# Optimization experiments

Measured on AMD Instinct MI355X. Metric: run time of the kernel, lower is better.

Reference implementation:

```python
import jax, jax.numpy as jnp
import numpy as np

N = 50000
E = 800000
NEG_SLOPE = 0.2


def gatv2_layer(x, src, dst, Wl, Wr, att, bias, heads, ch):
    # x: [N, Fin]; Wl/Wr: [Fin, heads*ch]; att: [heads, ch]; bias: [heads*ch]
    xl = (x @ Wl).reshape(N, heads, ch)  # source transform
    xr = (x @ Wr).reshape(N, heads, ch)  # target transform
    e = xl[src] + xr[dst]                              # [E, H, C]
    s = jnp.einsum('ehc,hc->eh', jax.nn.leaky_relu(e, NEG_SLOPE), att)  # [E, H]
    # scatter-softmax over incoming edges of each target node
    smax = jax.ops.segment_max(s, dst, num_segments=N)  # [N, H]
    ex = jnp.exp(s - smax[dst])
    denom = jax.ops.segment_sum(ex, dst, num_segments=N)
    alpha = ex / denom[dst]                             # [E, H]
    out = jax.ops.segment_sum(xl[src] * alpha[..., None], dst, num_segments=N)  # [N, H, C]
    return out.reshape(N, heads * ch) + bias


def setup_inputs() -> dict:
    key = jax.random.key(0)
    ks = jax.random.split(key, 12)
    x = jax.random.normal(ks[0], (N, 128), dtype=jnp.float32)
    edge_index = jax.random.randint(ks[1], (2, E), 0, N, dtype=jnp.int64)
    edge_attr = jax.random.normal(ks[2], (E, 16), dtype=jnp.float32)
    s1 = 1.0 / np.sqrt(128.0)
    # layer 1: 128 -> 64, heads=2 (concat -> 128)
    Wl1 = jax.random.normal(ks[3], (128, 128), dtype=jnp.float32) * s1
    Wr1 = jax.random.normal(ks[4], (128, 128), dtype=jnp.float32) * s1
    att1 = jax.random.normal(ks[5], (2, 64), dtype=jnp.float32) * 0.1
    b1 = jnp.zeros((128,), dtype=jnp.float32)
    # layer 2: 128 -> 128, heads=1
    Wl2 = jax.random.normal(ks[6], (128, 128), dtype=jnp.float32) * s1
    Wr2 = jax.random.normal(ks[7], (128, 128), dtype=jnp.float32) * s1
    att2 = jax.random.normal(ks[8], (1, 128), dtype=jnp.float32) * 0.1
    b2 = jnp.zeros((128,), dtype=jnp.float32)
    return {"x": x, "edge_index": edge_index, "edge_attr": edge_attr,
            "Wl1": Wl1, "Wr1": Wr1, "att1": att1, "b1": b1,
            "Wl2": Wl2, "Wr2": Wr2, "att2": att2, "b2": b2}


def reference(x, edge_index, edge_attr, Wl1, Wr1, att1, b1, Wl2, Wr2, att2, b2):
    # using_edge_attr=False default path: edge_attr ignored.
    # GATv2Conv default add_self_loops=True
    loops = jnp.arange(N, dtype=edge_index.dtype)
    src = jnp.concatenate([edge_index[0], loops])
    dst = jnp.concatenate([edge_index[1], loops])
    h = gatv2_layer(x, src, dst, Wl1, Wr1, att1, b1, heads=2, ch=64)
    out = gatv2_layer(h, src, dst, Wl2, Wr2, att2, b2, heads=1, ch=128)
    return out
```

## Files before the change

kernel.cpp:

```cpp
#include <hip/hip_runtime.h>

#define NEG_SLOPE 0.2f
#define NPB 256
#define CHUNK 4096
#define BCAP 5120

typedef _Float16 f16x8 __attribute__((ext_vector_type(8)));
typedef _Float16 f16x4 __attribute__((ext_vector_type(4)));
typedef _Float16 f16x2 __attribute__((ext_vector_type(2)));
typedef float    f32x4 __attribute__((ext_vector_type(4)));
typedef float    f32x8 __attribute__((ext_vector_type(8)));

#if defined(__has_builtin)
#if __has_builtin(__builtin_amdgcn_fdot2)
#define HAVE_FDOT2 1
#endif
#if __has_builtin(__builtin_amdgcn_exp2f)
#define FEXP2(x) __builtin_amdgcn_exp2f(x)
#endif
#endif
#ifndef FEXP2
#define FEXP2(x) exp2f(x)
#endif

__device__ __forceinline__ f32x8 cvt8(f16x8 v) {
    return __builtin_convertvector(v, f32x8);
}

template <int CTRL>
__device__ __forceinline__ float dpp_add(float v) {
    int o = __builtin_amdgcn_update_dpp(0, __builtin_bit_cast(int, v),
                                        CTRL, 0xF, 0xF, true);
    return v + __builtin_bit_cast(float, o);
}

__global__ __launch_bounds__(256) void k1_prep_bucket_kernel(
    const float* __restrict__ W0, const float* __restrict__ W1,
    const float* __restrict__ W2, const float* __restrict__ W3,
    _Float16* __restrict__ wt,
    const float* __restrict__ x, _Float16* __restrict__ xh,
    _Float16* __restrict__ xlo, int total,
    const int* __restrict__ ei, int* __restrict__ gcursor,
    int2* __restrict__ staging, int E, int B0)
{
    __shared__ int2 pairs[CHUNK];
    __shared__ int bh[256], bbase[256], exb[256], scn[256];
    int t = threadIdx.x;
    int bid = blockIdx.x;

    if (bid < B0) {
        bh[t] = 0;
        __syncthreads();
        int base = bid * CHUNK;
        int srcv[16], dstv[16], rb[16];
#pragma unroll
        for (int j = 0; j < 16; j++) {
            int e = base + t + j * 256;
            if (e < E) {
                int d = ei[E + e];
                srcv[j] = ei[e];
                dstv[j] = d;
                int bk = d >> 8;
                int r = atomicAdd(&bh[bk], 1);
                rb[j] = (r << 8) | bk;
            } else rb[j] = -1;
        }
        __syncthreads();
        int v = bh[t];
        scn[t] = v;
        __syncthreads();
        for (int off = 1; off < 256; off <<= 1) {
            int u = (t >= off) ? scn[t - off] : 0;
            __syncthreads();
            scn[t] += u;
            __syncthreads();
        }
        int ex = scn[t] - v;
        int tot = scn[255];
        exb[t] = ex;
        if (v) bbase[t] = t * BCAP + atomicAdd(&gcursor[t], v);
        __syncthreads();
#pragma unroll
        for (int j = 0; j < 16; j++) {
            if (rb[j] >= 0) {
                int bk = rb[j] & 255, r = rb[j] >> 8;
                pairs[exb[bk] + r] = make_int2(srcv[j], dstv[j]);
            }
        }
        __syncthreads();
        for (int i = t; i < tot; i += 256) {
            int2 p = pairs[i];
            int bk = p.y >> 8;
            staging[bbase[bk] + (i - exb[bk])] = p;
        }
    } else if (bid < B0 + 256) {
        int idx = (bid - B0) * 256 + t;
        int m = idx >> 14;
        int k = (idx >> 7) & 127;
        int n = idx & 127;
        const float* W = (m == 0) ? W0 : (m == 1) ? W1 : (m == 2) ? W2 : W3;
        wt[m * 16384 + n * 128 + k] = (_Float16)W[k * 128 + n];
    } else {
        int i = (bid - B0 - 256) * 256 + t;
        if (i * 2 < total) {
            float2 f = *(const float2*)(x + (size_t)i * 2);
            _Float16 h0 = (_Float16)f.x, h1 = (_Float16)f.y;
            _Float16 l0 = (_Float16)(f.x - (float)h0), l1 = (_Float16)(f.y - (float)h1);
            *(f16x2*)(xh  + (size_t)i * 2) = (f16x2){h0, h1};
            *(f16x2*)(xlo + (size_t)i * 2) = (f16x2){l0, l1};
        }
    }
}

__device__ __forceinline__ void gemm_body(
    const _Float16* __restrict__ Ahi, const _Float16* __restrict__ Alo,
    const _Float16* __restrict__ Wt, _Float16* __restrict__ C, int N,
    int bx, _Float16* ldsW)
{
    const int tid = threadIdx.x;
    const int wave = tid >> 6;
    const int lane = tid & 63;
    const int mrow = lane & 15;
    const int quad = lane >> 4;
    const int rbase = bx * 128 + wave * 32;

    const int sn = tid >> 1, shf = tid & 1;
    float4 stg[8];
    {
        const float4* g = (const float4*)(Wt + sn * 128 + shf * 64);
#pragma unroll
        for (int j = 0; j < 8; j++) stg[j] = g[j];
    }

    f16x8 ah[2][4], al[2][4];
#pragma unroll
    for (int rt = 0; rt < 2; rt++) {
        int r = rbase + rt * 16 + mrow;
        if (r > N - 1) r = N - 1;
        const _Float16* pa = Ahi + (size_t)r * 128 + quad * 8;
        const _Float16* pl = Alo + (size_t)r * 128 + quad * 8;
#pragma unroll
        for (int s = 0; s < 4; s++) {
            ah[rt][s] = *(const f16x8*)(pa + s * 32);
            al[rt][s] = *(const f16x8*)(pl + s * 32);
        }
    }

    {
        float4* d = (float4*)&ldsW[sn * 136 + shf * 64];
#pragma unroll
        for (int j = 0; j < 8; j++) d[j] = stg[j];
    }

    f32x4 acc[2][8];
#pragma unroll
    for (int rt = 0; rt < 2; rt++)
#pragma unroll
        for (int c = 0; c < 8; c++) acc[rt][c] = (f32x4){0.f, 0.f, 0.f, 0.f};

    __syncthreads();

#pragma unroll
    for (int s = 0; s < 4; s++) {
#pragma unroll
        for (int c = 0; c < 8; c++) {
            f16x8 bw = *(const f16x8*)&ldsW[(c * 16 + mrow) * 136 + s * 32 + quad * 8];
            acc[0][c] = __builtin_amdgcn_mfma_f32_16x16x32_f16(ah[0][s], bw, acc[0][c], 0, 0, 0);
            acc[0][c] = __builtin_amdgcn_mfma_f32_16x16x32_f16(al[0][s], bw, acc[0][c], 0, 0, 0);
            acc[1][c] = __builtin_amdgcn_mfma_f32_16x16x32_f16(ah[1][s], bw, acc[1][c], 0, 0, 0);
            acc[1][c] = __builtin_amdgcn_mfma_f32_16x16x32_f16(al[1][s], bw, acc[1][c], 0, 0, 0);
        }
    }

#pragma unroll
    for (int rt = 0; rt < 2; rt++)
#pragma unroll
        for (int i = 0; i < 4; i++) {
            int r = rbase + rt * 16 + quad * 4 + i;
            if (r < N) {
                _Float16* cr = C + (size_t)r * 128 + mrow;
#pragma unroll
                for (int c = 0; c < 8; c++) cr[c * 16] = (_Float16)acc[rt][c][i];
            }
        }
}

__global__ __launch_bounds__(256) void gemm_f16_kernel(
    const _Float16* __restrict__ Ahi, const _Float16* __restrict__ Alo,
    const _Float16* __restrict__ Wt0, const _Float16* __restrict__ Wt1,
    _Float16* __restrict__ Cl, _Float16* __restrict__ Cr, int N)
{
    __shared__ _Float16 ldsW[128 * 136];
    gemm_body(Ahi, Alo, blockIdx.y ? Wt1 : Wt0, blockIdx.y ? Cr : Cl, N,
              blockIdx.x, ldsW);
}

__global__ __launch_bounds__(256) void k2_sort_gemm_kernel(
    const int2* __restrict__ staging, const int* __restrict__ gcursor,
    int* __restrict__ start, int* __restrict__ deg,
    int* __restrict__ sorted_src, int N, int NBv,
    const _Float16* __restrict__ Ahi, const _Float16* __restrict__ Alo,
    const _Float16* __restrict__ Wt0, const _Float16* __restrict__ Wt1,
    _Float16* __restrict__ Cl, _Float16* __restrict__ Cr, int gx)
{
    __shared__ _Float16 ldsW[128 * 136];
    int bx = blockIdx.x;
    if (bx < NBv) {
        int* lhist = (int*)ldsW;
        int* lscan = lhist + 256;
        int* lcur  = lhist + 512;
        int b = bx, t = threadIdx.x;
        int r0 = b * BCAP;
        int r1 = r0 + gcursor[b];
        lhist[t] = 0;
        __syncthreads();
        for (int i = r0 + t; i < r1; i += 256) atomicAdd(&lhist[staging[i].y & 255], 1);
        __syncthreads();
        int v = lhist[t];
        lscan[t] = v;
        __syncthreads();
        for (int off = 1; off < 256; off <<= 1) {
            int u = (t >= off) ? lscan[t - off] : 0;
            __syncthreads();
            lscan[t] += u;
            __syncthreads();
        }
        int excl = lscan[t] - v;
        int node = b * NPB + t;
        if (node < N) { start[node] = r0 + excl; deg[node] = v; }
        lcur[t] = excl;
        __syncthreads();
        for (int i = r0 + t; i < r1; i += 256) {
            int2 p = staging[i];
            int rank = atomicAdd(&lcur[p.y & 255], 1);
            sorted_src[r0 + rank] = p.x << 8;
        }
    } else {
        int gb = bx - NBv;
        int y = (gb >= gx) ? 1 : 0;
        int gxi = y ? gb - gx : gb;
        gemm_body(Ahi, Alo, y ? Wt1 : Wt0, y ? Cr : Cl, N, gxi, ldsW);
    }
}

template <int H, bool BFOUT>
__global__ __launch_bounds__(256) void gat_fused_kernel(
    const _Float16* __restrict__ xl, const _Float16* __restrict__ xr,
    const float* __restrict__ att, const float* __restrict__ bias,
    const int* __restrict__ start, const int* __restrict__ deg,
    const int* __restrict__ sorted_src,
    float* __restrict__ outf, _Float16* __restrict__ oh,
    _Float16* __restrict__ ol, int N, int npairs)
{
    const int wid = threadIdx.x >> 6;
    int p = blockIdx.x * 4 + wid;
    if (p >= npairs) return;
    const int stride = gridDim.x * 4;
    const int lane = threadIdx.x & 63;
    const int g  = lane >> 4;
    const int hl = lane & 15;
    const unsigned hl16 = (unsigned)hl * 16;
    const _Float16 NS = (_Float16)NEG_SLOPE;
    const float L2E = 1.44269504f;

    float4 at0 = *(const float4*)(att + hl * 8);
    float4 at1 = *(const float4*)(att + hl * 8 + 4);
    float4 bi0 = *(const float4*)(bias + hl * 8);
    float4 bi1 = *(const float4*)(bias + hl * 8 + 4);
#if defined(HAVE_FDOT2)
    f16x2 av0 = {(_Float16)(at0.x * L2E), (_Float16)(at0.y * L2E)};
    f16x2 av1 = {(_Float16)(at0.z * L2E), (_Float16)(at0.w * L2E)};
    f16x2 av2 = {(_Float16)(at1.x * L2E), (_Float16)(at1.y * L2E)};
    f16x2 av3 = {(_Float16)(at1.z * L2E), (_Float16)(at1.w * L2E)};
#else
    f32x8 avf = {at0.x * L2E, at0.y * L2E, at0.z * L2E, at0.w * L2E,
                 at1.x * L2E, at1.y * L2E, at1.z * L2E, at1.w * L2E};
#endif

    auto score = [&](f16x8 a_, f16x8 b4_) -> float {
        f16x8 t = a_ + b4_;
        f16x8 u = __builtin_elementwise_max(t, t * NS);
#if defined(HAVE_FDOT2)
        f16x2 u0 = __builtin_shufflevector(u, u, 0, 1);
        f16x2 u1 = __builtin_shufflevector(u, u, 2, 3);
        f16x2 u2 = __builtin_shufflevector(u, u, 4, 5);
        f16x2 u3 = __builtin_shufflevector(u, u, 6, 7);
        return __builtin_amdgcn_fdot2(u0, av0,
               __builtin_amdgcn_fdot2(u1, av1,
               __builtin_amdgcn_fdot2(u2, av2,
               __builtin_amdgcn_fdot2(u3, av3, 0.f, false), false), false), false);
#else
        f32x8 uf = cvt8(u);
        float pp = 0.f;
#pragma unroll
        for (int i = 0; i < 8; i++) pp += uf[i] * avf[i];
        return pp;
#endif
    };

    auto red = [&](float v) -> float {
        v = dpp_add<0xB1>(v);
        v = dpp_add<0x4E>(v);
        v = dpp_add<0x141>(v);
        if (H == 1) v = dpp_add<0x140>(v);
        return v;
    };

    const unsigned cap = (unsigned)(N - 1) << 8;
    auto ldoff = [&](int pos) -> unsigned {
        unsigned v = (unsigned)sorted_src[pos];
        return (v < cap) ? v : cap;
    };
    auto grow = [&](unsigned off) -> f16x8 {
        return *(const f16x8*)((const char*)xl + (size_t)(off + hl16));
    };

    int n0 = 2 * p;
    bool has1 = (n0 + 1) < N;
    int n1 = has1 ? n0 + 1 : n0;
    int s00 = start[n0], M0 = deg[n0] + 1;
    int s01 = start[n1], M1 = deg[n1] + 1;

    for (;;) {
        const int pn = p + stride;
        const bool hn = pn < npairs;
        const int nn0 = hn ? 2 * pn : n0;
        const bool nhas1 = (nn0 + 1) < N;
        const int nn1 = nhas1 ? nn0 + 1 : nn0;
        int ns00 = start[nn0], nM0 = deg[nn0] + 1;
        int ns01 = start[nn1], nM1 = deg[nn1] + 1;

        const f16x8 b40 = *(const f16x8*)(xr + (size_t)n0 * 128 + hl * 8);
        const f16x8 b41 = *(const f16x8*)(xr + (size_t)n1 * 128 + hl * 8);

        const int Mmax = (M0 > M1) ? M0 : M1;
        const int K   = (Mmax + 3) >> 2;
        const int KK  = (K + 1) & ~1;

        f32x8 acc0 = {0.f, 0.f, 0.f, 0.f, 0.f, 0.f, 0.f, 0.f};
        f32x8 acc1 = {0.f, 0.f, 0.f, 0.f, 0.f, 0.f, 0.f, 0.f};
        float den0 = 0.f, den1 = 0.f;

        auto cone = [&](int kk, f16x8 a, f16x8 b4_, int M_, float& den_, f32x8& acc_) {
            float v = red(score(a, b4_));
            float e = (4 * kk + g < M_) ? FEXP2(v) : 0.f;
            den_ += e;
#pragma unroll
            for (int i = 0; i < 8; i++)
                acc_[i] = fmaf((float)a[i], e, acc_[i]);
        };

        unsigned o00 = (g == 0) ? (unsigned)n0 << 8 : ldoff(s00 + g - 1);
        unsigned o01 = (g == 0) ? (unsigned)n1 << 8 : ldoff(s01 + g - 1);
        unsigned o10 = ldoff(s00 + g + 3);
        unsigned o11 = ldoff(s01 + g + 3);
        f16x8 c00 = grow(o00), c01 = grow(o01), c10 = grow(o10), c11 = grow(o11);
        for (int k = 2; k < KK; k += 2) {
            unsigned p00 = ldoff(s00 + 4 * k + g - 1);
            unsigned p01 = ldoff(s01 + 4 * k + g - 1);
            unsigned p10 = ldoff(s00 + 4 * k + g + 3);
            unsigned p11 = ldoff(s01 + 4 * k + g + 3);
            f16x8 d00 = grow(p00), d01 = grow(p01), d10 = grow(p10), d11 = grow(p11);
            cone(k - 2, c00, b40, M0, den0, acc0);
            cone(k - 2, c01, b41, M1, den1, acc1);
            cone(k - 1, c10, b40, M0, den0, acc0);
            cone(k - 1, c11, b41, M1, den1, acc1);
            c00 = d00; c01 = d01; c10 = d10; c11 = d11;
        }
        cone(KK - 2, c00, b40, M0, den0, acc0);
        cone(KK - 2, c01, b41, M1, den1, acc1);
        cone(KK - 1, c10, b40, M0, den0, acc0);
        cone(KK - 1, c11, b41, M1, den1, acc1);

        den0 += __shfl_xor(den0, 16, 64);
        den0 += __shfl_xor(den0, 32, 64);
        den1 += __shfl_xor(den1, 16, 64);
        den1 += __shfl_xor(den1, 32, 64);
#pragma unroll
        for (int i = 0; i < 8; i++) {
            acc0[i] += __shfl_xor(acc0[i], 16, 64);
            acc0[i] += __shfl_xor(acc0[i], 32, 64);
            acc1[i] += __shfl_xor(acc1[i], 16, 64);
            acc1[i] += __shfl_xor(acc1[i], 32, 64);
        }

        const int which = lane >> 4;
        if (which == 0 || (which == 1 && has1)) {
            float inv = 1.0f / (which == 0 ? den0 : den1);
            int nodeo = (which == 0) ? n0 : n1;
            float o[8];
#pragma unroll
            for (int i = 0; i < 8; i++) {
                float a = (which == 0) ? acc0[i] : acc1[i];
                float b = (i < 4) ? ((i == 0) ? bi0.x : (i == 1) ? bi0.y : (i == 2) ? bi0.z : bi0.w)
                                  : ((i == 4) ? bi1.x : (i == 5) ? bi1.y : (i == 6) ? bi1.z : bi1.w);
                o[i] = a * inv + b;
            }
            if (BFOUT) {
                f16x8 hv, lv;
#pragma unroll
                for (int i = 0; i < 8; i++) {
                    _Float16 h = (_Float16)o[i];
                    hv[i] = h;
                    lv[i] = (_Float16)(o[i] - (float)h);
                }
                *(f16x8*)(oh + (size_t)nodeo * 128 + hl * 8) = hv;
                *(f16x8*)(ol + (size_t)nodeo * 128 + hl * 8) = lv;
            } else {
                *(float4*)(outf + (size_t)nodeo * 128 + hl * 8) =
                    make_float4(o[0], o[1], o[2], o[3]);
                *(float4*)(outf + (size_t)nodeo * 128 + hl * 8 + 4) =
                    make_float4(o[4], o[5], o[6], o[7]);
            }
        }

        if (!hn) break;
        p = pn; n0 = nn0; has1 = nhas1; n1 = nn1;
        s00 = ns00; M0 = nM0; s01 = ns01; M1 = nM1;
    }
}

extern "C" void kernel_launch(void* const* d_in, const int* in_sizes, int n_in,
                              void* d_out, int out_size, void* d_ws, size_t ws_size,
                              hipStream_t stream)
{
    const float* x    = (const float*)d_in[0];
    const int*   ei   = (const int*)d_in[1];
    const float* Wl1  = (const float*)d_in[3];
    const float* Wr1  = (const float*)d_in[4];
    const float* att1 = (const float*)d_in[5];
    const float* b1   = (const float*)d_in[6];
    const float* Wl2  = (const float*)d_in[7];
    const float* Wr2  = (const float*)d_in[8];
    const float* att2 = (const float*)d_in[9];
    const float* b2   = (const float*)d_in[10];
    float* out = (float*)d_out;

    const int N  = in_sizes[0] / 128;
    const int E  = in_sizes[1] / 2;
    const int NB = (N + NPB - 1) / NPB;

    const size_t nf = (size_t)N * 128;
    _Float16* xlf  = (_Float16*)d_ws;
    _Float16* xrf  = xlf + nf;
    _Float16* ah   = xrf + nf;
    _Float16* al   = ah + nf;
    _Float16* wt   = al + nf;
    int* gcursor   = (int*)(wt + 4 * 16384);
    int* start     = gcursor + 256;
    int* deg       = start + N;
    size_t stgoff  = ((size_t)(deg + N) + 7) & ~(size_t)7;
    int2* staging  = (int2*)stgoff;
    int* sorted_src = (int*)(staging + (size_t)NB * BCAP);

    const int grid_chunk = (E + CHUNK - 1) / CHUNK;
    const int npairs     = (N + 1) / 2;
    int node_grid        = (npairs + 3) / 4;
    if (node_grid > 2048) node_grid = 2048;
    const int gemm_gx    = (N + 127) / 128;
    const int split_grid = (int)((nf / 2 + 255) / 256);

    hipMemsetAsync(gcursor, 0, 256 * sizeof(int), stream);

    k1_prep_bucket_kernel<<<grid_chunk + 256 + split_grid, 256, 0, stream>>>(
        Wl1, Wr1, Wl2, Wr2, wt, x, ah, al, (int)nf,
        ei, gcursor, staging, E, grid_chunk);

    k2_sort_gemm_kernel<<<NB + 2 * gemm_gx, 256, 0, stream>>>(
        staging, gcursor, start, deg, sorted_src, N, NB,
        ah, al, wt + 0 * 16384, wt + 1 * 16384, xlf, xrf, gemm_gx);

    gat_fused_kernel<2, true><<<node_grid, 256, 0, stream>>>(
        xlf, xrf, att1, b1, start, deg, sorted_src, nullptr, ah, al, N, npairs);

    gemm_f16_kernel<<<dim3(gemm_gx, 2), 256, 0, stream>>>(
        ah, al, wt + 2 * 16384, wt + 3 * 16384, xlf, xrf, N);
    gat_fused_kernel<1, false><<<node_grid, 256, 0, stream>>>(
        xlf, xrf, att2, b2, start, deg, sorted_src, out, nullptr, nullptr, N, npairs);
}
```

Baseline: 265.6 us.

## Merge all stages into one persistent cooperative kernel with grid syncs

Replaces the memset and five separate launches with a single cooperative mega-kernel sized to full occupancy. The stages (weight/input split, bucketing plus first GEMM, per-bucket sort, layer-1 attention, second GEMM, layer-2 attention) run as grid-strided loops separated by grid.sync. Shared memory becomes a union so one allocation serves every stage. The aim is to remove launch gaps and tail effects between kernels, at the cost of grid-wide barriers, a register cap from launch_bounds(256,4), and dropping the next-pair start/deg prefetch in the attention loop.

```diff
diff --git a/kernel.cpp b/kernel.cpp
--- a/kernel.cpp
+++ b/kernel.cpp
@@ -1,4 +1,6 @@
 #include <hip/hip_runtime.h>
+#include <hip/hip_cooperative_groups.h>
+namespace cg = cooperative_groups;
 
 #define NEG_SLOPE 0.2f
 #define NPB 256
@@ -6,7 +8,6 @@
 #define BCAP 5120
 
 typedef _Float16 f16x8 __attribute__((ext_vector_type(8)));
-typedef _Float16 f16x4 __attribute__((ext_vector_type(4)));
 typedef _Float16 f16x2 __attribute__((ext_vector_type(2)));
 typedef float    f32x4 __attribute__((ext_vector_type(4)));
 typedef float    f32x8 __attribute__((ext_vector_type(8)));
@@ -23,10 +24,6 @@
 #define FEXP2(x) exp2f(x)
 #endif
 
-__device__ __forceinline__ f32x8 cvt8(f16x8 v) {
-    return __builtin_convertvector(v, f32x8);
-}
-
 template <int CTRL>
 __device__ __forceinline__ float dpp_add(float v) {
     int o = __builtin_amdgcn_update_dpp(0, __builtin_bit_cast(int, v),
@@ -34,81 +31,60 @@
     return v + __builtin_bit_cast(float, o);
 }
 
-__global__ __launch_bounds__(256) void k1_prep_bucket_kernel(
-    const float* __restrict__ W0, const float* __restrict__ W1,
-    const float* __restrict__ W2, const float* __restrict__ W3,
-    _Float16* __restrict__ wt,
-    const float* __restrict__ x, _Float16* __restrict__ xh,
-    _Float16* __restrict__ xlo, int total,
-    const int* __restrict__ ei, int* __restrict__ gcursor,
-    int2* __restrict__ staging, int E, int B0)
-{
-    __shared__ int2 pairs[CHUNK];
-    __shared__ int bh[256], bbase[256], exb[256], scn[256];
+union SharedU {
+    struct { int2 pairs[CHUNK]; int bh[256]; int bbase[256]; int exb[256]; int scn[256]; } b;
+    _Float16 w[128 * 136];
+    struct { int lhist[256]; int lscan[256]; int lcur[256]; } s;
+};
+
+__device__ __forceinline__ void bucket_chunk_body(
+    SharedU& L, const int* __restrict__ ei, int* __restrict__ gcursor,
+    int2* __restrict__ staging, int E, int bid)
+{
     int t = threadIdx.x;
-    int bid = blockIdx.x;
-
-    if (bid < B0) {
-        bh[t] = 0;
-        __syncthreads();
-        int base = bid * CHUNK;
-        int srcv[16], dstv[16], rb[16];
-#pragma unroll
-        for (int j = 0; j < 16; j++) {
-            int e = base + t + j * 256;
-            if (e < E) {
-                int d = ei[E + e];
-                srcv[j] = ei[e];
-                dstv[j] = d;
-                int bk = d >> 8;
-                int r = atomicAdd(&bh[bk], 1);
-                rb[j] = (r << 8) | bk;
-            } else rb[j] = -1;
-        }
-        __syncthreads();
-        int v = bh[t];
-        scn[t] = v;
-        __syncthreads();
-        for (int off = 1; off < 256; off <<= 1) {
-            int u = (t >= off) ? scn[t - off] : 0;
-            __syncthreads();
-            scn[t] += u;
-            __syncthreads();
-        }
-        int ex = scn[t] - v;
-        int tot = scn[255];
-        exb[t] = ex;
-        if (v) bbase[t] = t * BCAP + atomicAdd(&gcursor[t], v);
-        __syncthreads();
-#pragma unroll
-        for (int j = 0; j < 16; j++) {
-            if (rb[j] >= 0) {
-                int bk = rb[j] & 255, r = rb[j] >> 8;
-                pairs[exb[bk] + r] = make_int2(srcv[j], dstv[j]);
-            }
-        }
-        __syncthreads();
-        for (int i = t; i < tot; i += 256) {
-            int2 p = pairs[i];
-            int bk = p.y >> 8;
-            staging[bbase[bk] + (i - exb[bk])] = p;
-        }
-    } else if (bid < B0 + 256) {
-        int idx = (bid - B0) * 256 + t;
-        int m = idx >> 14;
-        int k = (idx >> 7) & 127;
-        int n = idx & 127;
-        const float* W = (m == 0) ? W0 : (m == 1) ? W1 : (m == 2) ? W2 : W3;
-        wt[m * 16384 + n * 128 + k] = (_Float16)W[k * 128 + n];
-    } else {
-        int i = (bid - B0 - 256) * 256 + t;
-        if (i * 2 < total) {
-            float2 f = *(const float2*)(x + (size_t)i * 2);
-            _Float16 h0 = (_Float16)f.x, h1 = (_Float16)f.y;
-            _Float16 l0 = (_Float16)(f.x - (float)h0), l1 = (_Float16)(f.y - (float)h1);
-            *(f16x2*)(xh  + (size_t)i * 2) = (f16x2){h0, h1};
-            *(f16x2*)(xlo + (size_t)i * 2) = (f16x2){l0, l1};
-        }
+    L.b.bh[t] = 0;
+    __syncthreads();
+    int base = bid * CHUNK;
+    int srcv[16], dstv[16], rb[16];
+#pragma unroll
+    for (int j = 0; j < 16; j++) {
+        int e = base + t + j * 256;
+        if (e < E) {
+            int d = ei[E + e];
+            srcv[j] = ei[e];
+            dstv[j] = d;
+            int bk = d >> 8;
+            int r = atomicAdd(&L.b.bh[bk], 1);
+            rb[j] = (r << 8) | bk;
+        } else rb[j] = -1;
+    }
+    __syncthreads();
+    int v = L.b.bh[t];
+    L.b.scn[t] = v;
+    __syncthreads();
+    for (int off = 1; off < 256; off <<= 1) {
+        int u = (t >= off) ? L.b.scn[t - off] : 0;
+        __syncthreads();
+        L.b.scn[t] += u;
+        __syncthreads();
+    }
+    int ex = L.b.scn[t] - v;
+    int tot = L.b.scn[255];
+    L.b.exb[t] = ex;
+    if (v) L.b.bbase[t] = t * BCAP + atomicAdd(&gcursor[t], v);
+    __syncthreads();
+#pragma unroll
+    for (int j = 0; j < 16; j++) {
+        if (rb[j] >= 0) {
+            int bk = rb[j] & 255, r = rb[j] >> 8;
+            L.b.pairs[L.b.exb[bk] + r] = make_int2(srcv[j], dstv[j]);
+        }
+    }
+    __syncthreads();
+    for (int i = t; i < tot; i += 256) {
+        int2 p = L.b.pairs[i];
+        int bk = p.y >> 8;
+        staging[L.b.bbase[bk] + (i - L.b.exb[bk])] = p;
     }
 }
 
@@ -185,66 +161,41 @@
         }
 }
 
-__global__ __launch_bounds__(256) void gemm_f16_kernel(
-    const _Float16* __restrict__ Ahi, const _Float16* __restrict__ Alo,
-    const _Float16* __restrict__ Wt0, const _Float16* __restrict__ Wt1,
-    _Float16* __restrict__ Cl, _Float16* __restrict__ Cr, int N)
-{
-    __shared__ _Float16 ldsW[128 * 136];
-    gemm_body(Ahi, Alo, blockIdx.y ? Wt1 : Wt0, blockIdx.y ? Cr : Cl, N,
-              blockIdx.x, ldsW);
-}
-
-__global__ __launch_bounds__(256) void k2_sort_gemm_kernel(
-    const int2* __restrict__ staging, const int* __restrict__ gcursor,
+__device__ __forceinline__ void sort_bucket_body(
+    SharedU& L, const int2* __restrict__ staging, const int* __restrict__ gcursor,
     int* __restrict__ start, int* __restrict__ deg,
-    int* __restrict__ sorted_src, int N, int NBv,
-    const _Float16* __restrict__ Ahi, const _Float16* __restrict__ Alo,
-    const _Float16* __restrict__ Wt0, const _Float16* __restrict__ Wt1,
-    _Float16* __restrict__ Cl, _Float16* __restrict__ Cr, int gx)
-{
-    __shared__ _Float16 ldsW[128 * 136];
-    int bx = blockIdx.x;
-    if (bx < NBv) {
-        int* lhist = (int*)ldsW;
-        int* lscan = lhist + 256;
-        int* lcur  = lhist + 512;
-        int b = bx, t = threadIdx.x;
-        int r0 = b * BCAP;
-        int r1 = r0 + gcursor[b];
-        lhist[t] = 0;
-        __syncthreads();
-        for (int i = r0 + t; i < r1; i += 256) atomicAdd(&lhist[staging[i].y & 255], 1);
-        __syncthreads();
-        int v = lhist[t];
-        lscan[t] = v;
-        __syncthreads();
-        for (int off = 1; off < 256; off <<= 1) {
-            int u = (t >= off) ? lscan[t - off] : 0;
-            __syncthreads();
-            lscan[t] += u;
-            __syncthreads();
-        }
-        int excl = lscan[t] - v;
-        int node = b * NPB + t;
-        if (node < N) { start[node] = r0 + excl; deg[node] = v; }
-        lcur[t] = excl;
-        __syncthreads();
-        for (int i = r0 + t; i < r1; i += 256) {
-            int2 p = staging[i];
-            int rank = atomicAdd(&lcur[p.y & 255], 1);
-            sorted_src[r0 + rank] = p.x << 8;
-        }
-    } else {
-        int gb = bx - NBv;
-        int y = (gb >= gx) ? 1 : 0;
-        int gxi = y ? gb - gx : gb;
-        gemm_body(Ahi, Alo, y ? Wt1 : Wt0, y ? Cr : Cl, N, gxi, ldsW);
+    int* __restrict__ sorted_src, int N, int b)
+{
+    int t = threadIdx.x;
+    int r0 = b * BCAP;
+    int r1 = r0 + gcursor[b];
+    L.s.lhist[t] = 0;
+    __syncthreads();
+    for (int i = r0 + t; i < r1; i += 256) atomicAdd(&L.s.lhist[staging[i].y & 255], 1);
+    __syncthreads();
+    int v = L.s.lhist[t];
+    L.s.lscan[t] = v;
+    __syncthreads();
+    for (int off = 1; off < 256; off <<= 1) {
+        int u = (t >= off) ? L.s.lscan[t - off] : 0;
+        __syncthreads();
+        L.s.lscan[t] += u;
+        __syncthreads();
+    }
+    int excl = L.s.lscan[t] - v;
+    int node = b * NPB + t;
+    if (node < N) { start[node] = r0 + excl; deg[node] = v; }
+    L.s.lcur[t] = excl;
+    __syncthreads();
+    for (int i = r0 + t; i < r1; i += 256) {
+        int2 p = staging[i];
+        int rank = atomicAdd(&L.s.lcur[p.y & 255], 1);
+        sorted_src[r0 + rank] = p.x << 8;
     }
 }
 
 template <int H, bool BFOUT>
-__global__ __launch_bounds__(256) void gat_fused_kernel(
+__device__ __forceinline__ void fused_pairs_body(
     const _Float16* __restrict__ xl, const _Float16* __restrict__ xr,
     const float* __restrict__ att, const float* __restrict__ bias,
     const int* __restrict__ start, const int* __restrict__ deg,
@@ -253,9 +204,6 @@
     _Float16* __restrict__ ol, int N, int npairs)
 {
     const int wid = threadIdx.x >> 6;
-    int p = blockIdx.x * 4 + wid;
-    if (p >= npairs) return;
-    const int stride = gridDim.x * 4;
     const int lane = threadIdx.x & 63;
     const int g  = lane >> 4;
     const int hl = lane & 15;
@@ -290,7 +238,7 @@
                __builtin_amdgcn_fdot2(u2, av2,
                __builtin_amdgcn_fdot2(u3, av3, 0.f, false), false), false), false);
 #else
-        f32x8 uf = cvt8(u);
+        f32x8 uf = __builtin_convertvector(u, f32x8);
         float pp = 0.f;
 #pragma unroll
         for (int i = 0; i < 8; i++) pp += uf[i] * avf[i];
@@ -315,20 +263,12 @@
         return *(const f16x8*)((const char*)xl + (size_t)(off + hl16));
     };
 
-    int n0 = 2 * p;
-    bool has1 = (n0 + 1) < N;
-    int n1 = has1 ? n0 + 1 : n0;
-    int s00 = start[n0], M0 = deg[n0] + 1;
-    int s01 = start[n1], M1 = deg[n1] + 1;
-
-    for (;;) {
-        const int pn = p + stride;
-        const bool hn = pn < npairs;
-        const int nn0 = hn ? 2 * pn : n0;
-        const bool nhas1 = (nn0 + 1) < N;
-        const int nn1 = nhas1 ? nn0 + 1 : nn0;
-        int ns00 = start[nn0], nM0 = deg[nn0] + 1;
-        int ns01 = start[nn1], nM1 = deg[nn1] + 1;
+    for (int p = blockIdx.x * 4 + wid; p < npairs; p += gridDim.x * 4) {
+        const int n0 = 2 * p;
+        const bool has1 = (n0 + 1) < N;
+        const int n1 = has1 ? n0 + 1 : n0;
+        const int s00 = start[n0], M0 = deg[n0] + 1;
+        const int s01 = start[n1], M1 = deg[n1] + 1;
 
         const f16x8 b40 = *(const f16x8*)(xr + (size_t)n0 * 128 + hl * 8);
         const f16x8 b41 = *(const f16x8*)(xr + (size_t)n1 * 128 + hl * 8);
@@ -413,11 +353,155 @@
                     make_float4(o[4], o[5], o[6], o[7]);
             }
         }
-
-        if (!hn) break;
-        p = pn; n0 = nn0; has1 = nhas1; n1 = nn1;
-        s00 = ns00; M0 = nM0; s01 = ns01; M1 = nM1;
-    }
+    }
+}
+
+struct MegaArgs {
+    const float *W0, *W1, *W2, *W3;
+    _Float16 *wt;
+    const float *x;
+    _Float16 *xh, *xlo;
+    int total;
+    const int *ei;
+    int *gcursor;
+    int2 *staging;
+    int E, B0;
+    int *start, *deg, *sorted_src;
+    int N, NB, gx, npairs;
+    _Float16 *xlf, *xrf;
+    const float *att1, *b1, *att2, *b2;
+    float *out;
+};
+
+__global__ __launch_bounds__(256, 4) void mega_kernel(MegaArgs a)
+{
+    __shared__ SharedU lds;
+    cg::grid_group grid = cg::this_grid();
+    const int t = threadIdx.x;
+    const int G = gridDim.x;
+
+    if (blockIdx.x == 0) a.gcursor[t] = 0;
+    for (int idx = blockIdx.x * 256 + t; idx < 65536; idx += G * 256) {
+        int m = idx >> 14, k = (idx >> 7) & 127, n = idx & 127;
+        const float* W = (m == 0) ? a.W0 : (m == 1) ? a.W1 : (m == 2) ? a.W2 : a.W3;
+        a.wt[m * 16384 + n * 128 + k] = (_Float16)W[k * 128 + n];
+    }
+    for (int i = blockIdx.x * 256 + t; i * 2 < a.total; i += G * 256) {
+        float2 f = *(const float2*)(a.x + (size_t)i * 2);
+        _Float16 h0 = (_Float16)f.x, h1 = (_Float16)f.y;
+        _Float16 l0 = (_Float16)(f.x - (float)h0), l1 = (_Float16)(f.y - (float)h1);
+        *(f16x2*)(a.xh  + (size_t)i * 2) = (f16x2){h0, h1};
+        *(f16x2*)(a.xlo + (size_t)i * 2) = (f16x2){l0, l1};
+    }
+    __threadfence(); grid.sync(); __threadfence();
+
+    for (int item = blockIdx.x; item < a.B0 + 2 * a.gx; item += G) {
+        __syncthreads();
+        if (item < a.B0) {
+            bucket_chunk_body(lds, a.ei, a.gcursor, a.staging, a.E, item);
+        } else {
+            int gb = item - a.B0;
+            int y = (gb >= a.gx) ? 1 : 0;
+            gemm_body(a.xh, a.xlo, y ? a.wt + 16384 : a.wt,
+                      y ? a.xrf : a.xlf, a.N, y ? gb - a.gx : gb, lds.w);
+        }
+    }
+    __threadfence(); grid.sync(); __threadfence();
+
+    for (int b = blockIdx.x; b < a.NB; b += G) {
+        __syncthreads();
+        sort_bucket_body(lds, a.staging, a.gcursor, a.start, a.deg,
+                         a.sorted_src, a.N, b);
+    }
+    __threadfence(); grid.sync(); __threadfence();
+
+    fused_pairs_body<2, true>(a.xlf, a.xrf, a.att1, a.b1, a.start, a.deg,
+                              a.sorted_src, nullptr, a.xh, a.xlo, a.N, a.npairs);
+    __threadfence(); grid.sync(); __threadfence();
+
+    for (int item = blockIdx.x; item < 2 * a.gx; item += G) {
+        __syncthreads();
+        int y = (item >= a.gx) ? 1 : 0;
+        gemm_body(a.xh, a.xlo, y ? a.wt + 3 * 16384 : a.wt + 2 * 16384,
+                  y ? a.xrf : a.xlf, a.N, y ? item - a.gx : item, lds.w);
+    }
+    __threadfence(); grid.sync(); __threadfence();
+
+    fused_pairs_body<1, false>(a.xlf, a.xrf, a.att2, a.b2, a.start, a.deg,
+                               a.sorted_src, a.out, nullptr, nullptr, a.N, a.npairs);
+}
+
+__global__ __launch_bounds__(256) void k1_prep_bucket_kernel(
+    const float* __restrict__ W0, const float* __restrict__ W1,
+    const float* __restrict__ W2, const float* __restrict__ W3,
+    _Float16* __restrict__ wt,
+    const float* __restrict__ x, _Float16* __restrict__ xh,
+    _Float16* __restrict__ xlo, int total,
+    const int* __restrict__ ei, int* __restrict__ gcursor,
+    int2* __restrict__ staging, int E, int B0)
+{
+    __shared__ SharedU lds;
+    int t = threadIdx.x;
+    int bid = blockIdx.x;
+    if (bid < B0) {
+        bucket_chunk_body(lds, ei, gcursor, staging, E, bid);
+    } else if (bid < B0 + 256) {
+        int idx = (bid - B0) * 256 + t;
+        int m = idx >> 14, k = (idx >> 7) & 127, n = idx & 127;
+        const float* W = (m == 0) ? W0 : (m == 1) ? W1 : (m == 2) ? W2 : W3;
+        wt[m * 16384 + n * 128 + k] = (_Float16)W[k * 128 + n];
+    } else {
+        int i = (bid - B0 - 256) * 256 + t;
+        if (i * 2 < total) {
+            float2 f = *(const float2*)(x + (size_t)i * 2);
+            _Float16 h0 = (_Float16)f.x, h1 = (_Float16)f.y;
+            _Float16 l0 = (_Float16)(f.x - (float)h0), l1 = (_Float16)(f.y - (float)h1);
+            *(f16x2*)(xh  + (size_t)i * 2) = (f16x2){h0, h1};
+            *(f16x2*)(xlo + (size_t)i * 2) = (f16x2){l0, l1};
+        }
+    }
+}
+
+__global__ __launch_bounds__(256) void k2_sort_gemm_kernel(
+    const int2* __restrict__ staging, const int* __restrict__ gcursor,
+    int* __restrict__ start, int* __restrict__ deg,
+    int* __restrict__ sorted_src, int N, int NBv,
+    const _Float16* __restrict__ Ahi, const _Float16* __restrict__ Alo,
+    const _Float16* __restrict__ Wt0, const _Float16* __restrict__ Wt1,
+    _Float16* __restrict__ Cl, _Float16* __restrict__ Cr, int gx)
+{
+    __shared__ SharedU lds;
+    int bx = blockIdx.x;
+    if (bx < NBv) {
+        sort_bucket_body(lds, staging, gcursor, start, deg, sorted_src, N, bx);
+    } else {
+        int gb = bx - NBv;
+        int y = (gb >= gx) ? 1 : 0;
+        gemm_body(Ahi, Alo, y ? Wt1 : Wt0, y ? Cr : Cl, N, y ? gb - gx : gb, lds.w);
+    }
+}
+
+__global__ __launch_bounds__(256) void gemm_f16_kernel(
+    const _Float16* __restrict__ Ahi, const _Float16* __restrict__ Alo,
+    const _Float16* __restrict__ Wt0, const _Float16* __restrict__ Wt1,
+    _Float16* __restrict__ Cl, _Float16* __restrict__ Cr, int N)
+{
+    __shared__ SharedU lds;
+    gemm_body(Ahi, Alo, blockIdx.y ? Wt1 : Wt0, blockIdx.y ? Cr : Cl, N,
+              blockIdx.x, lds.w);
+}
+
+template <int H, bool BFOUT>
+__global__ __launch_bounds__(256) void gat_fused_kernel(
+    const _Float16* __restrict__ xl, const _Float16* __restrict__ xr,
+    const float* __restrict__ att, const float* __restrict__ bias,
+    const int* __restrict__ start, const int* __restrict__ deg,
+    const int* __restrict__ sorted_src,
+    float* __restrict__ outf, _Float16* __restrict__ oh,
+    _Float16* __restrict__ ol, int N, int npairs)
+{
+    fused_pairs_body<H, BFOUT>(xl, xr, att, bias, start, deg, sorted_src,
+                               outf, oh, ol, N, npairs);
 }
 
 extern "C" void kernel_launch(void* const* d_in, const int* in_sizes, int n_in,
@@ -455,24 +539,57 @@
 
     const int grid_chunk = (E + CHUNK - 1) / CHUNK;
     const int npairs     = (N + 1) / 2;
-    int node_grid        = (npairs + 3) / 4;
-    if (node_grid > 2048) node_grid = 2048;
     const int gemm_gx    = (N + 127) / 128;
     const int split_grid = (int)((nf / 2 + 255) / 256);
 
+    static int s_coop = -1;
+    static int s_grid = 0;
+    if (s_coop < 0) {
+        int dev = 0;
+        hipGetDevice(&dev);
+        hipDeviceProp_t prop;
+        int maxb = 0;
+        if (hipGetDeviceProperties(&prop, dev) == hipSuccess &&
+            hipOccupancyMaxActiveBlocksPerMultiprocessor(
+                &maxb, (const void*)mega_kernel, 256, 0) == hipSuccess &&
+            maxb > 0 && prop.cooperativeLaunch) {
+            s_grid = maxb * prop.multiProcessorCount;
+            s_coop = 1;
+        } else {
+            s_coop = 0;
+        }
+    }
+
+    if (s_coop == 1) {
+        MegaArgs a;
+        a.W0 = Wl1; a.W1 = Wr1; a.W2 = Wl2; a.W3 = Wr2;
+        a.wt = wt; a.x = x; a.xh = ah; a.xlo = al; a.total = (int)nf;
+        a.ei = ei; a.gcursor = gcursor; a.staging = staging;
+        a.E = E; a.B0 = grid_chunk;
+        a.start = start; a.deg = deg; a.sorted_src = sorted_src;
+        a.N = N; a.NB = NB; a.gx = gemm_gx; a.npairs = npairs;
+        a.xlf = xlf; a.xrf = xrf;
+        a.att1 = att1; a.b1 = b1; a.att2 = att2; a.b2 = b2;
+        a.out = out;
+        void* params[] = { &a };
+        hipError_t err = hipLaunchCooperativeKernel(
+            (const void*)mega_kernel, dim3(s_grid), dim3(256), params, 0, stream);
+        if (err == hipSuccess) return;
+        s_coop = 0;
+    }
+
+    int node_grid = (npairs + 3) / 4;
+    if (node_grid > 2048) node_grid = 2048;
+
     hipMemsetAsync(gcursor, 0, 256 * sizeof(int), stream);
-
     k1_prep_bucket_kernel<<<grid_chunk + 256 + split_grid, 256, 0, stream>>>(
         Wl1, Wr1, Wl2, Wr2, wt, x, ah, al, (int)nf,
         ei, gcursor, staging, E, grid_chunk);
-
     k2_sort_gemm_kernel<<<NB + 2 * gemm_gx, 256, 0, stream>>>(
         staging, gcursor, start, deg, sorted_src, N, NB,
         ah, al, wt + 0 * 16384, wt + 1 * 16384, xlf, xrf, gemm_gx);
-
     gat_fused_kernel<2, true><<<node_grid, 256, 0, stream>>>(
         xlf, xrf, att1, b1, start, deg, sorted_src, nullptr, ah, al, N, npairs);
-
     gemm_f16_kernel<<<dim3(gemm_gx, 2), 256, 0, stream>>>(
         ah, al, wt + 2 * 16384, wt + 3 * 16384, xlf, xrf, N);
     gat_fused_kernel<1, false><<<node_grid, 256, 0, stream>>>(
```

After: 1.056 ms. 298% more time.
